# Kernel optimization log

Hardware: AMD Instinct MI355X
Metric: run time of the kernel (lower is better)

Reference implementation:

```python
import jax, jax.numpy as jnp
import numpy as np

V, E, H, T = 100000, 128, 256, 7
B, S = 64, 512
START, STOP = 5, 6
H2 = H // 2


def setup_inputs() -> dict:
    key = jax.random.key(0)
    ks = jax.random.split(key, 16)
    rn = lambda k, shape, s=0.1: jax.random.normal(k, shape, jnp.float32) * s
    inp = {}
    inp["sentence"] = jax.random.randint(ks[0], (B, S), 0, V)
    inp["tags"] = jax.random.randint(ks[1], (B, S), 0, 5)
    inp["h0"] = jax.random.normal(ks[2], (2, B, H2), jnp.float32)
    inp["c0"] = jax.random.normal(ks[3], (2, B, H2), jnp.float32)
    inp["embedding"] = rn(ks[4], (V, E), 1.0)
    inp["w_ih_f"] = rn(ks[5], (4 * H2, E)); inp["w_hh_f"] = rn(ks[6], (4 * H2, H2))
    inp["b_ih_f"] = rn(ks[7], (4 * H2,)); inp["b_hh_f"] = rn(ks[8], (4 * H2,))
    inp["w_ih_b"] = rn(ks[9], (4 * H2, E)); inp["w_hh_b"] = rn(ks[10], (4 * H2, H2))
    inp["b_ih_b"] = rn(ks[11], (4 * H2,)); inp["b_hh_b"] = rn(ks[12], (4 * H2,))
    inp["w_out"] = rn(ks[13], (T, H)); inp["b_out"] = rn(ks[14], (T,))
    trans = jax.random.normal(ks[15], (T, T), jnp.float32)
    trans = trans.at[START, :].set(-10000.0).at[:, STOP].set(-10000.0)
    inp["transitions"] = trans
    return inp


def _lstm_dir(x, h0, c0, wih, whh, bih, bhh, reverse):
    # x: [S, B, E]; PyTorch gate order i, f, g, o
    def step(carry, xt):
        h, c = carry
        z = xt @ wih.T + h @ whh.T + bih + bhh  # [B, 4*H2]
        i, f, g, o = jnp.split(z, 4, axis=-1)
        c = jax.nn.sigmoid(f) * c + jax.nn.sigmoid(i) * jnp.tanh(g)
        h = jax.nn.sigmoid(o) * jnp.tanh(c)
        return (h, c), h
    _, hs = jax.lax.scan(step, (h0, c0), x, reverse=reverse)
    return hs  # [S, B, H2]


def reference(sentence, tags, h0, c0, embedding, w_ih_f, w_hh_f, b_ih_f, b_hh_f,
              w_ih_b, w_hh_b, b_ih_b, b_hh_b, w_out, b_out, transitions):
    # Embedding; torch code does .view(S, B, -1) on a [B, S, E] tensor (raw
    # reinterpretation) -- replicate with reshape to match the math exactly.
    embeds = embedding[sentence].reshape(S, B, E)
    hf = _lstm_dir(embeds, h0[0], c0[0], w_ih_f, w_hh_f, b_ih_f, b_hh_f, False)
    hb = _lstm_dir(embeds, h0[1], c0[1], w_ih_b, w_hh_b, b_ih_b, b_hh_b, True)
    feats = jnp.concatenate([hf, hb], axis=-1) @ w_out.T + b_out  # [S, B, T]

    # CRF forward algorithm. Original uses transitions.t(), i.e. step score
    # for prev=i -> next=j is transitions[i, j].
    alpha0 = jnp.full((B, T), -10000.0, jnp.float32).at[:, START].set(0.0)
    def crf_step(alpha, feat):
        # [b, i, j]: alpha[b,i] + transitions[i,j]; LSE over i, add emit[b,j]
        a = jax.nn.logsumexp(alpha[:, :, None] + transitions[None, :, :], axis=1) + feat
        return a, None
    alpha, _ = jax.lax.scan(crf_step, alpha0, feats)
    fwd_score = jax.nn.logsumexp(alpha + transitions[STOP][None, :], axis=1)  # [B]

    # Gold path score: transitions[next, prev] + emit[next], per _score_sentence.
    tags_ext = jnp.concatenate([jnp.full((B, 1), START, tags.dtype), tags], axis=1)
    t_prev, t_next = tags_ext[:, :-1], tags_ext[:, 1:]  # [B, S]
    trans_sc = transitions[t_next, t_prev].sum(axis=1)
    emit_sc = jnp.take_along_axis(jnp.transpose(feats, (1, 0, 2)),
                                  t_next[:, :, None], axis=2)[..., 0].sum(axis=1)
    gold = trans_sc + emit_sc + transitions[STOP, tags_ext[:, -1]]
    return jnp.sum(fwd_score - gold) / B
```

## Files before the change

kernel.cpp:

```cpp
#include <hip/hip_runtime.h>

typedef unsigned int u32;
typedef unsigned short u16;
typedef __attribute__((ext_vector_type(8))) short short8;
typedef __attribute__((ext_vector_type(4))) float f32x4;

#define DEV __device__ __forceinline__
#define LOG2E 1.44269504089f

DEV u16 f2bf(float f) {
    u32 u = __float_as_uint(f);
    return (u16)((u + 0x7FFFu + ((u >> 16) & 1u)) >> 16);
}
DEV float bf2f(u16 h) { return __uint_as_float(((u32)h) << 16); }
DEV float frcp(float x) { return __builtin_amdgcn_rcpf(x); }
DEV float fexp2(float x) {
#if __has_builtin(__builtin_amdgcn_exp2f)
    return __builtin_amdgcn_exp2f(x);
#else
    return exp2f(x);
#endif
}
DEV u32 pack_bf16(float a, float b) {
#if __has_builtin(__builtin_amdgcn_cvt_pk_bf16_f32)
    auto v = __builtin_amdgcn_cvt_pk_bf16_f32(a, b);
    u32 r; __builtin_memcpy(&r, &v, 4); return r;
#else
    return (u32)f2bf(a) | ((u32)f2bf(b) << 16);
#endif
}
DEV float xex(uint2 v, int r) {
    u32 u = (r & 2) ? v.y : v.x;
    return (r & 1) ? __uint_as_float(u & 0xFFFF0000u) : __uint_as_float(u << 16);
}

__global__ __launch_bounds__(512) void k_inproj2(
    const int* __restrict__ sent, const float* __restrict__ emb,
    const float* __restrict__ wihf, const float* __restrict__ bihf, const float* __restrict__ bhhf,
    const float* __restrict__ wihb, const float* __restrict__ bihb, const float* __restrict__ bhhb,
    u16* __restrict__ Xf, u16* __restrict__ Xb)
{
    int blk = blockIdx.x;
    int d  = blk >> 8;
    int g4 = (blk >> 6) & 3;
    int sc = blk & 63;
    const float* wih = d ? wihb : wihf;
    const float* bih = d ? bihb : bihf;
    const float* bhh = d ? bhhb : bhhf;
    u16* X = d ? Xb : Xf;
    int tid = threadIdx.x;
    int w = tid >> 6, lane = tid & 63;
    int rg = lane >> 4, cn = lane & 15;

    short8 afr[4][4];
    #pragma unroll
    for (int mi = 0; mi < 4; ++mi) {
        int gate = 16 * (w + 8 * mi) + cn;
        #pragma unroll
        for (int kt = 0; kt < 4; ++kt) {
            const float* p = wih + (size_t)gate * 128 + kt * 32 + rg * 8;
            float4 f0 = *(const float4*)p;
            float4 f1 = *(const float4*)(p + 4);
            union { short8 v; u32 u[4]; } sv;
            sv.u[0] = pack_bf16(f0.x, f0.y);
            sv.u[1] = pack_bf16(f0.z, f0.w);
            sv.u[2] = pack_bf16(f1.x, f1.y);
            sv.u[3] = pack_bf16(f1.z, f1.w);
            afr[mi][kt] = sv.v;
        }
    }
    float bs[4][4];
    #pragma unroll
    for (int mi = 0; mi < 4; ++mi)
        #pragma unroll
        for (int r = 0; r < 4; ++r) {
            int g = 16 * (w + 8 * mi) + 4 * rg + r;
            bs[mi][r] = bih[g] + bhh[g];
        }

    __shared__ int toks[128];
    __shared__ u16 tile[8][16][136];
    if (tid < 128)
        toks[tid] = sent[(sc * 8 + (tid >> 4)) * 64 + g4 * 16 + (tid & 15)];
    __syncthreads();
    {
        int rr = tid >> 2, q = tid & 3;
        int ss = rr >> 4, nn = rr & 15;
        const float* er = emb + (size_t)toks[rr] * 128 + q * 32;
        u16* dst = &tile[ss][nn][q * 32];
        #pragma unroll
        for (int u = 0; u < 4; ++u) {
            float4 a = *(const float4*)(er + u * 8);
            float4 c = *(const float4*)(er + u * 8 + 4);
            uint4 st;
            st.x = pack_bf16(a.x, a.y); st.y = pack_bf16(a.z, a.w);
            st.z = pack_bf16(c.x, c.y); st.w = pack_bf16(c.z, c.w);
            *(uint4*)(dst + u * 8) = st;
        }
    }
    __syncthreads();

    for (int ss = 0; ss < 8; ++ss) {
        short8 bfr[4];
        #pragma unroll
        for (int kt = 0; kt < 4; ++kt)
            bfr[kt] = *(const short8*)&tile[ss][cn][kt * 32 + rg * 8];
        int s = sc * 8 + ss;
        #pragma unroll
        for (int mi = 0; mi < 4; ++mi) {
            f32x4 acc = {0.f, 0.f, 0.f, 0.f};
            #pragma unroll
            for (int kt = 0; kt < 4; ++kt)
                acc = __builtin_amdgcn_mfma_f32_16x16x32_bf16(afr[mi][kt], bfr[kt], acc, 0, 0, 0);
            size_t base = (((size_t)s * 4 + g4) * 32 + (w + 8 * mi)) * 256
                        + (size_t)rg * 64 + (size_t)cn * 4;
            uint2 st;
            st.x = pack_bf16((acc[0] + bs[mi][0]) * LOG2E, (acc[1] + bs[mi][1]) * LOG2E);
            st.y = pack_bf16((acc[2] + bs[mi][2]) * LOG2E, (acc[3] + bs[mi][3]) * LOG2E);
            *(uint2*)(X + base) = st;
        }
    }
}

__global__ __launch_bounds__(512) void k_lstm(
    const float* __restrict__ h0, const float* __restrict__ c0,
    const float* __restrict__ whhf, const float* __restrict__ whhb,
    const u16* __restrict__ Xf, const u16* __restrict__ Xb,
    u16* __restrict__ hfo, u16* __restrict__ hbo)
{
    int d  = blockIdx.x >> 2, g4 = blockIdx.x & 3;
    const float* whh = d ? whhb : whhf;
    const u16*   X   = d ? Xb   : Xf;
    u16*         ho  = d ? hbo  : hfo;
    int w = threadIdx.x >> 6, lane = threadIdx.x & 63;
    int rg = lane >> 4, cn = lane & 15;

    short8 afr[4][4];
    #pragma unroll
    for (int mi = 0; mi < 4; ++mi) {
        int gate = 16 * (w + 8 * mi) + cn;
        #pragma unroll
        for (int kt = 0; kt < 4; ++kt) {
            const float* p = whh + (size_t)gate * 128 + kt * 32 + rg * 8;
            float4 f0 = *(const float4*)p;
            float4 f1 = *(const float4*)(p + 4);
            union { short8 v; u32 u[4]; } sv;
            sv.u[0] = pack_bf16(f0.x * LOG2E, f0.y * LOG2E);
            sv.u[1] = pack_bf16(f0.z * LOG2E, f0.w * LOG2E);
            sv.u[2] = pack_bf16(f1.x * LOG2E, f1.y * LOG2E);
            sv.u[3] = pack_bf16(f1.z * LOG2E, f1.w * LOG2E);
            afr[mi][kt] = sv.v;
        }
    }
    int b = g4 * 16 + cn;
    int chb = 16 * w + rg * 4;
    float cst[4];
    {
        float4 cv = *(const float4*)(c0 + ((size_t)d * 64 + b) * 128 + chb);
        cst[0]=cv.x; cst[1]=cv.y; cst[2]=cv.z; cst[3]=cv.w;
    }
    __shared__ u16 hbuf[2][16][136];
    {
        float4 hv = *(const float4*)(h0 + ((size_t)d * 64 + b) * 128 + chb);
        uint2 st0;
        st0.x = pack_bf16(hv.x, hv.y);
        st0.y = pack_bf16(hv.z, hv.w);
        *(uint2*)&hbuf[0][cn][chb] = st0;
    }
    __syncthreads();

    int s0 = d ? 511 : 0;
    const int sdelta = d ? -32768 : 32768;
    const ptrdiff_t hdelta = d ? -8192 : 8192;
    size_t lof = (size_t)rg * 64 + (size_t)cn * 4;

    const u16* pa[4]; const u16* pb[4];
    uint2 xA[4], xB[4];
    #pragma unroll
    for (int mi = 0; mi < 4; ++mi) {
        const u16* base = X + (((size_t)s0 * 4 + g4) * 32 + (w + 8 * mi)) * 256 + lof;
        xA[mi] = *(const uint2*)base;
        xB[mi] = *(const uint2*)(base + sdelta);
        pa[mi] = base + 2 * sdelta;
        pb[mi] = base + 3 * sdelta;
    }
    u16* hop = ho + ((size_t)s0 * 64 + b) * 128 + chb;

#define LSTM_STEP(RB, WB, XC, XP)                                            \
    do {                                                                     \
        short8 bfr[4];                                                       \
        _Pragma("unroll")                                                    \
        for (int kt = 0; kt < 4; ++kt)                                       \
            bfr[kt] = *(const short8*)&hbuf[RB][cn][kt * 32 + rg * 8];       \
        f32x4 z[4];                                                          \
        _Pragma("unroll")                                                    \
        for (int mi = 0; mi < 4; ++mi) {                                     \
            f32x4 acc;                                                       \
            acc[0] = xex(XC[mi], 0); acc[1] = xex(XC[mi], 1);                \
            acc[2] = xex(XC[mi], 2); acc[3] = xex(XC[mi], 3);                \
            _Pragma("unroll")                                                \
            for (int kt = 0; kt < 4; ++kt)                                   \
                acc = __builtin_amdgcn_mfma_f32_16x16x32_bf16(               \
                    afr[mi][kt], bfr[kt], acc, 0, 0, 0);                     \
            z[mi] = acc;                                                     \
            XC[mi] = *(const uint2*)XP[mi];                                  \
            XP[mi] += 2 * sdelta;                                            \
        }                                                                    \
        float hnew[4];                                                       \
        _Pragma("unroll")                                                    \
        for (int r = 0; r < 4; ++r) {                                        \
            float zi = z[0][r], zf = z[1][r], zg = z[2][r], zo = z[3][r];    \
            float ei = fexp2(-zi);                                           \
            float ef = fexp2(-zf);                                           \
            float eo = fexp2(-zo);                                           \
            float eg = fexp2(fminf(zg + zg, 115.f));                         \
            float A = 1.f + ei, F = 1.f + ef, G = eg + 1.f, O = 1.f + eo;    \
            float AG = A * G;                                                \
            float cc = (cst[r] * AG + (eg - 1.f) * F) * frcp(F * AG);        \
            cst[r] = cc;                                                     \
            float ec = fexp2(fminf(2.885390082f * cc, 115.f));               \
            hnew[r] = (ec - 1.f) * frcp(O * (ec + 1.f));                     \
        }                                                                    \
        uint2 st;                                                            \
        st.x = pack_bf16(hnew[0], hnew[1]);                                  \
        st.y = pack_bf16(hnew[2], hnew[3]);                                  \
        *(uint2*)&hbuf[WB][cn][chb] = st;                                    \
        *(uint2*)hop = st;                                                   \
        hop += hdelta;                                                       \
        asm volatile("s_waitcnt lgkmcnt(0)\n\ts_barrier" ::: "memory");      \
    } while (0)

    for (int it = 0; it < 256; ++it) {
        LSTM_STEP(0, 1, xA, pa);
        LSTM_STEP(1, 0, xB, pb);
    }
#undef LSTM_STEP
}

__global__ __launch_bounds__(256) void k_feats(
    const u16* __restrict__ hf, const u16* __restrict__ hb,
    const float* __restrict__ wout, const float* __restrict__ bout,
    float* __restrict__ feats)
{
    __shared__ u16 sf[32][136], sb[32][136];
    __shared__ float wo[7][260];
    __shared__ float bo[8];
    int tid = threadIdx.x;
    int pos0 = blockIdx.x * 32;
    {
        int r = tid >> 3, cc = (tid & 7) * 16;
        const uint4* pf = (const uint4*)(hf + (size_t)(pos0 + r) * 128 + cc);
        const uint4* pb = (const uint4*)(hb + (size_t)(pos0 + r) * 128 + cc);
        *(uint4*)&sf[r][cc]     = pf[0];
        *(uint4*)&sf[r][cc + 8] = pf[1];
        *(uint4*)&sb[r][cc]     = pb[0];
        *(uint4*)&sb[r][cc + 8] = pb[1];
    }
    for (int i = tid; i < 1792; i += 256) wo[i >> 8][i & 255] = wout[i];
    if (tid < 7) bo[tid] = bout[tid];
    __syncthreads();
    int pp = tid >> 3, tt = tid & 7;
    if (tt < 7) {
        float acc = bo[tt];
        #pragma unroll 4
        for (int ch = 0; ch < 128; ++ch)
            acc += bf2f(sf[pp][ch]) * wo[tt][ch]
                 + bf2f(sb[pp][ch]) * wo[tt][128 + ch];
        feats[(size_t)(pos0 + pp) * 7 + tt] = acc;
    }
}

__global__ __launch_bounds__(64) void k_crf_chunk(
    const float* __restrict__ feats, const float* __restrict__ trans,
    float* __restrict__ chunkM)
{
    int b = blockIdx.x >> 3, c = blockIdx.x & 7;
    int lane = threadIdx.x;
    int i = lane >> 3, j = lane & 7;
    __shared__ float M[8][8];
    __shared__ float fl[64][8];
    int s0 = c * 64;
    for (int idx = lane; idx < 448; idx += 64) {
        int ss = idx / 7, jj = idx - ss * 7;
        fl[ss][jj] = feats[(size_t)((s0 + ss) * 64 + b) * 7 + jj];
    }
    float tc[7];
    #pragma unroll
    for (int k = 0; k < 7; ++k) tc[k] = (j < 7) ? trans[k * 7 + j] : 0.f;
    __syncthreads();
    M[i][j] = (i < 7 && j < 7) ? (trans[i * 7 + j] + fl[0][j]) : -1e30f;
    __syncthreads();
    for (int ss = 1; ss < 64; ++ss) {
        float4 m0 = *(const float4*)&M[i][0];
        float4 m1 = *(const float4*)&M[i][4];
        float v0 = m0.x + tc[0], v1 = m0.y + tc[1], v2 = m0.z + tc[2];
        float v3 = m0.w + tc[3], v4 = m1.x + tc[4], v5 = m1.y + tc[5];
        float v6 = m1.z + tc[6];
        float mx = fmaxf(fmaxf(fmaxf(v0, v1), fmaxf(v2, v3)),
                         fmaxf(fmaxf(v4, v5), v6));
        float sm = __expf(v0 - mx) + __expf(v1 - mx) + __expf(v2 - mx)
                 + __expf(v3 - mx) + __expf(v4 - mx) + __expf(v5 - mx)
                 + __expf(v6 - mx);
        float r = mx + __logf(sm) + fl[ss][j];
        __syncthreads();
        if (i < 7 && j < 7) M[i][j] = r;
        __syncthreads();
    }
    if (i < 7 && j < 7)
        chunkM[(size_t)(b * 8 + c) * 49 + i * 7 + j] = M[i][j];
}

__global__ __launch_bounds__(64) void k_crf_final(
    const float* __restrict__ chunkM, const float* __restrict__ trans,
    const int* __restrict__ tags, const float* __restrict__ feats,
    float* __restrict__ out)
{
    int b = blockIdx.x;
    int lane = threadIdx.x;
    __shared__ float P[8][49];
    __shared__ float Tl[49];
    __shared__ float av[2][8];
    __shared__ int   tg[512];
    for (int idx = lane; idx < 392; idx += 64)
        P[idx / 49][idx % 49] = chunkM[(size_t)b * 392 + idx];
    if (lane < 49) Tl[lane] = trans[lane];
    for (int idx = lane; idx < 512; idx += 64) tg[idx] = tags[(size_t)b * 512 + idx];
    if (lane < 8) av[0][lane] = (lane == 5) ? 0.f : -1e4f;
    __syncthreads();
    int cur = 0;
    for (int cch = 0; cch < 8; ++cch) {
        if (lane < 7) {
            float vv[7], mx = -1e30f;
            #pragma unroll
            for (int ii = 0; ii < 7; ++ii) {
                vv[ii] = av[cur][ii] + P[cch][ii * 7 + lane];
                mx = fmaxf(mx, vv[ii]);
            }
            float sm = 0.f;
            #pragma unroll
            for (int ii = 0; ii < 7; ++ii) sm += __expf(vv[ii] - mx);
            av[cur ^ 1][lane] = mx + __logf(sm);
        }
        __syncthreads();
        cur ^= 1;
    }
    float mx = -1e30f, uu[7];
    #pragma unroll
    for (int jj = 0; jj < 7; ++jj) {
        uu[jj] = av[cur][jj] + Tl[6 * 7 + jj];
        mx = fmaxf(mx, uu[jj]);
    }
    float sm = 0.f;
    #pragma unroll
    for (int jj = 0; jj < 7; ++jj) sm += __expf(uu[jj] - mx);
    float fwd = mx + __logf(sm);
    float acc = 0.f;
    for (int ss = lane; ss < 512; ss += 64) {
        int tn = tg[ss];
        int tp = (ss == 0) ? 5 : tg[ss - 1];
        acc += Tl[tn * 7 + tp] + feats[(size_t)(ss * 64 + b) * 7 + tn];
    }
    #pragma unroll
    for (int mk = 32; mk >= 1; mk >>= 1) acc += __shfl_xor(acc, mk, 64);
    if (lane == 0) {
        float gold = acc + Tl[6 * 7 + tg[511]];
        atomicAdd(out, (fwd - gold) * (1.0f / 64.0f));
    }
}

extern "C" void kernel_launch(void* const* d_in, const int* in_sizes, int n_in,
                              void* d_out, int out_size, void* d_ws, size_t ws_size,
                              hipStream_t stream) {
    const int*   sent = (const int*)d_in[0];
    const int*   tags = (const int*)d_in[1];
    const float* h0   = (const float*)d_in[2];
    const float* c0   = (const float*)d_in[3];
    const float* emb  = (const float*)d_in[4];
    const float* wihf = (const float*)d_in[5];
    const float* whhf = (const float*)d_in[6];
    const float* bihf = (const float*)d_in[7];
    const float* bhhf = (const float*)d_in[8];
    const float* wihb = (const float*)d_in[9];
    const float* whhb = (const float*)d_in[10];
    const float* bihb = (const float*)d_in[11];
    const float* bhhb = (const float*)d_in[12];
    const float* wout = (const float*)d_in[13];
    const float* bout = (const float*)d_in[14];
    const float* trn  = (const float*)d_in[15];

    char* ws = (char*)d_ws;
    u16*   Xf     = (u16*)(ws);
    u16*   Xb     = (u16*)(ws + 33554432);
    u16*   hfp    = (u16*)(ws + 67108864);
    u16*   hbp    = (u16*)(ws + 75497472);
    float* feats  = (float*)(ws + 83886080);
    float* chunkM = (float*)(ws + 84803584);

    hipMemsetAsync(d_out, 0, 4, stream);
    k_inproj2<<<512, 512, 0, stream>>>(sent, emb, wihf, bihf, bhhf,
                                       wihb, bihb, bhhb, Xf, Xb);
    k_lstm<<<8, 512, 0, stream>>>(h0, c0, whhf, whhb, Xf, Xb, hfp, hbp);
    k_feats<<<1024, 256, 0, stream>>>(hfp, hbp, wout, bout, feats);
    k_crf_chunk<<<512, 64, 0, stream>>>(feats, trn, chunkM);
    k_crf_final<<<64, 64, 0, stream>>>(chunkM, trn, tags, feats, (float*)d_out);
}
```

Before: 576.8 us.

## Widen input-projection tiles to all batch columns and use scalar-base addressing in LSTM

The input projection kernel now has each block handle four timesteps across all 64 batch columns, in two staged 2-step shared tiles, instead of 8 timesteps for a 16-column group. This halves the grid so each block's W_ih fragment load and bf16 conversion is amortised over more MFMA work. The LSTM recurrence now uses a uniform scalar base pointer plus per-lane 32-bit offsets instead of per-lane 64-bit pointers, to cut address arithmetic and VGPR use on the serial critical path. The clamp limits and a couple of FMA contractions in the gate math are also tweaked. The risks are fewer blocks on the GPU and an extra barrier in the projection kernel.

```diff
diff --git a/kernel.cpp b/kernel.cpp
--- a/kernel.cpp
+++ b/kernel.cpp
@@ -41,9 +41,8 @@
     u16* __restrict__ Xf, u16* __restrict__ Xb)
 {
     int blk = blockIdx.x;
-    int d  = blk >> 8;
-    int g4 = (blk >> 6) & 3;
-    int sc = blk & 63;
+    int d  = blk >> 7;
+    int sc = blk & 127;
     const float* wih = d ? wihb : wihf;
     const float* bih = d ? bihb : bihf;
     const float* bhh = d ? bhhb : bhhf;
@@ -78,46 +77,50 @@
             bs[mi][r] = bih[g] + bhh[g];
         }
 
-    __shared__ int toks[128];
-    __shared__ u16 tile[8][16][136];
-    if (tid < 128)
-        toks[tid] = sent[(sc * 8 + (tid >> 4)) * 64 + g4 * 16 + (tid & 15)];
-    __syncthreads();
-    {
-        int rr = tid >> 2, q = tid & 3;
-        int ss = rr >> 4, nn = rr & 15;
-        const float* er = emb + (size_t)toks[rr] * 128 + q * 32;
-        u16* dst = &tile[ss][nn][q * 32];
+    __shared__ u16 tile[2][64][136];
+    #pragma unroll
+    for (int stage = 0; stage < 2; ++stage) {
+        if (stage) __syncthreads();
+        {
+            int row = tid >> 2, q = tid & 3;
+            int sl = row >> 6, bb = row & 63;
+            int tok = sent[(sc * 4 + stage * 2 + sl) * 64 + bb];
+            const float* er = emb + (size_t)tok * 128 + q * 32;
+            u16* dst = &tile[sl][bb][q * 32];
+            #pragma unroll
+            for (int u = 0; u < 4; ++u) {
+                float4 a = *(const float4*)(er + u * 8);
+                float4 c = *(const float4*)(er + u * 8 + 4);
+                uint4 st;
+                st.x = pack_bf16(a.x, a.y); st.y = pack_bf16(a.z, a.w);
+                st.z = pack_bf16(c.x, c.y); st.w = pack_bf16(c.z, c.w);
+                *(uint4*)(dst + u * 8) = st;
+            }
+        }
+        __syncthreads();
         #pragma unroll
-        for (int u = 0; u < 4; ++u) {
-            float4 a = *(const float4*)(er + u * 8);
-            float4 c = *(const float4*)(er + u * 8 + 4);
-            uint4 st;
-            st.x = pack_bf16(a.x, a.y); st.y = pack_bf16(a.z, a.w);
-            st.z = pack_bf16(c.x, c.y); st.w = pack_bf16(c.z, c.w);
-            *(uint4*)(dst + u * 8) = st;
-        }
-    }
-    __syncthreads();
-
-    for (int ss = 0; ss < 8; ++ss) {
-        short8 bfr[4];
-        #pragma unroll
-        for (int kt = 0; kt < 4; ++kt)
-            bfr[kt] = *(const short8*)&tile[ss][cn][kt * 32 + rg * 8];
-        int s = sc * 8 + ss;
-        #pragma unroll
-        for (int mi = 0; mi < 4; ++mi) {
-            f32x4 acc = {0.f, 0.f, 0.f, 0.f};
+        for (int ss = 0; ss < 2; ++ss) {
+            int s = sc * 4 + stage * 2 + ss;
             #pragma unroll
-            for (int kt = 0; kt < 4; ++kt)
-                acc = __builtin_amdgcn_mfma_f32_16x16x32_bf16(afr[mi][kt], bfr[kt], acc, 0, 0, 0);
-            size_t base = (((size_t)s * 4 + g4) * 32 + (w + 8 * mi)) * 256
-                        + (size_t)rg * 64 + (size_t)cn * 4;
-            uint2 st;
-            st.x = pack_bf16((acc[0] + bs[mi][0]) * LOG2E, (acc[1] + bs[mi][1]) * LOG2E);
-            st.y = pack_bf16((acc[2] + bs[mi][2]) * LOG2E, (acc[3] + bs[mi][3]) * LOG2E);
-            *(uint2*)(X + base) = st;
+            for (int nt = 0; nt < 4; ++nt) {
+                short8 bfr[4];
+                #pragma unroll
+                for (int kt = 0; kt < 4; ++kt)
+                    bfr[kt] = *(const short8*)&tile[ss][nt * 16 + cn][kt * 32 + rg * 8];
+                #pragma unroll
+                for (int mi = 0; mi < 4; ++mi) {
+                    f32x4 acc = {0.f, 0.f, 0.f, 0.f};
+                    #pragma unroll
+                    for (int kt = 0; kt < 4; ++kt)
+                        acc = __builtin_amdgcn_mfma_f32_16x16x32_bf16(afr[mi][kt], bfr[kt], acc, 0, 0, 0);
+                    size_t base = (((size_t)s * 4 + nt) * 32 + (w + 8 * mi)) * 256
+                                + (size_t)rg * 64 + (size_t)cn * 4;
+                    uint2 st;
+                    st.x = pack_bf16((acc[0] + bs[mi][0]) * LOG2E, (acc[1] + bs[mi][1]) * LOG2E);
+                    st.y = pack_bf16((acc[2] + bs[mi][2]) * LOG2E, (acc[3] + bs[mi][3]) * LOG2E);
+                    *(uint2*)(X + base) = st;
+                }
+            }
         }
     }
 }
@@ -170,23 +173,26 @@
     __syncthreads();
 
     int s0 = d ? 511 : 0;
-    const int sdelta = d ? -32768 : 32768;
-    const ptrdiff_t hdelta = d ? -8192 : 8192;
-    size_t lof = (size_t)rg * 64 + (size_t)cn * 4;
-
-    const u16* pa[4]; const u16* pb[4];
+    const int sdB = d ? -65536 : 65536;
+    const int hdB = d ? -16384 : 16384;
+
+    int voffB[4];
+    #pragma unroll
+    for (int mi = 0; mi < 4; ++mi)
+        voffB[mi] = 2 * ((w + 8 * mi) * 256 + rg * 64 + cn * 4);
+    const char* xbase = (const char*)X + ((size_t)s0 * 32768 + (size_t)g4 * 8192) * 2;
     uint2 xA[4], xB[4];
     #pragma unroll
     for (int mi = 0; mi < 4; ++mi) {
-        const u16* base = X + (((size_t)s0 * 4 + g4) * 32 + (w + 8 * mi)) * 256 + lof;
-        xA[mi] = *(const uint2*)base;
-        xB[mi] = *(const uint2*)(base + sdelta);
-        pa[mi] = base + 2 * sdelta;
-        pb[mi] = base + 3 * sdelta;
-    }
-    u16* hop = ho + ((size_t)s0 * 64 + b) * 128 + chb;
-
-#define LSTM_STEP(RB, WB, XC, XP)                                            \
+        xA[mi] = *(const uint2*)(xbase + voffB[mi]);
+        xB[mi] = *(const uint2*)(xbase + sdB + voffB[mi]);
+    }
+    const char* sxA = xbase + 2 * sdB;
+    const char* sxB = xbase + 3 * sdB;
+    int vhoff = 2 * (b * 128 + chb);
+    char* hsp = (char*)ho + (size_t)s0 * 16384;
+
+#define LSTM_STEP(RB, WB, XC, SX)                                            \
     do {                                                                     \
         short8 bfr[4];                                                       \
         _Pragma("unroll")                                                    \
@@ -203,9 +209,9 @@
                 acc = __builtin_amdgcn_mfma_f32_16x16x32_bf16(               \
                     afr[mi][kt], bfr[kt], acc, 0, 0, 0);                     \
             z[mi] = acc;                                                     \
-            XC[mi] = *(const uint2*)XP[mi];                                  \
-            XP[mi] += 2 * sdelta;                                            \
+            XC[mi] = *(const uint2*)(SX + voffB[mi]);                        \
         }                                                                    \
+        SX += 2 * sdB;                                                       \
         float hnew[4];                                                       \
         _Pragma("unroll")                                                    \
         for (int r = 0; r < 4; ++r) {                                        \
@@ -213,26 +219,27 @@
             float ei = fexp2(-zi);                                           \
             float ef = fexp2(-zf);                                           \
             float eo = fexp2(-zo);                                           \
-            float eg = fexp2(fminf(zg + zg, 115.f));                         \
-            float A = 1.f + ei, F = 1.f + ef, G = eg + 1.f, O = 1.f + eo;    \
+            float eg = fexp2(fminf(zg + zg, 126.f));                         \
+            float A = 1.f + ei, F = 1.f + ef, G = 1.f + eg, O = 1.f + eo;    \
             float AG = A * G;                                                \
-            float cc = (cst[r] * AG + (eg - 1.f) * F) * frcp(F * AG);        \
+            float num = fmaf(cst[r], AG, (eg - 1.f) * F);                    \
+            float cc  = num * frcp(F * AG);                                  \
             cst[r] = cc;                                                     \
-            float ec = fexp2(fminf(2.885390082f * cc, 115.f));               \
-            hnew[r] = (ec - 1.f) * frcp(O * (ec + 1.f));                     \
+            float ec = fexp2(fminf(2.885390082f * cc, 126.f));               \
+            hnew[r] = (ec - 1.f) * frcp(fmaf(O, ec, O));                     \
         }                                                                    \
         uint2 st;                                                            \
         st.x = pack_bf16(hnew[0], hnew[1]);                                  \
         st.y = pack_bf16(hnew[2], hnew[3]);                                  \
         *(uint2*)&hbuf[WB][cn][chb] = st;                                    \
-        *(uint2*)hop = st;                                                   \
-        hop += hdelta;                                                       \
+        *(uint2*)(hsp + vhoff) = st;                                         \
+        hsp += hdB;                                                          \
         asm volatile("s_waitcnt lgkmcnt(0)\n\ts_barrier" ::: "memory");      \
     } while (0)
 
     for (int it = 0; it < 256; ++it) {
-        LSTM_STEP(0, 1, xA, pa);
-        LSTM_STEP(1, 0, xB, pb);
+        LSTM_STEP(0, 1, xA, sxA);
+        LSTM_STEP(1, 0, xB, sxB);
     }
 #undef LSTM_STEP
 }
@@ -397,7 +404,7 @@
     float* chunkM = (float*)(ws + 84803584);
 
     hipMemsetAsync(d_out, 0, 4, stream);
-    k_inproj2<<<512, 512, 0, stream>>>(sent, emb, wihf, bihf, bhhf,
+    k_inproj2<<<256, 512, 0, stream>>>(sent, emb, wihf, bihf, bhhf,
                                        wihb, bihb, bhhb, Xf, Xb);
     k_lstm<<<8, 512, 0, stream>>>(h0, c0, whhf, whhb, Xf, Xb, hfp, hbp);
     k_feats<<<1024, 256, 0, stream>>>(hfp, hbp, wout, bout, feats);
```

Result: no change. 576.3 us (-0.1%).

## Retile input projection over full batch and fold CRF final into one block

Applied to the files above, without the earlier changes.

The input projection now has each block cover all 64 batch columns for 4 timesteps, in two staged halves, instead of 16 columns for 8 timesteps. This halves the grid and cuts how often each block's weight-fragment setup is repeated. The CRF final kernel becomes a single 512-thread block that runs all 64 batch rows with shuffles and reduces in shared memory, which removes the memset and the atomicAdd. The trade-off is fewer blocks for the projection and a serial per-thread gold-score loop over 64 steps. All of these kernels are small next to the sequential LSTM kernel.

```diff
diff --git a/kernel.cpp b/kernel.cpp
--- a/kernel.cpp
+++ b/kernel.cpp
@@ -41,9 +41,8 @@
     u16* __restrict__ Xf, u16* __restrict__ Xb)
 {
     int blk = blockIdx.x;
-    int d  = blk >> 8;
-    int g4 = (blk >> 6) & 3;
-    int sc = blk & 63;
+    int d  = blk >> 7;
+    int sc = blk & 127;
     const float* wih = d ? wihb : wihf;
     const float* bih = d ? bihb : bihf;
     const float* bhh = d ? bhhb : bhhf;
@@ -78,46 +77,50 @@
             bs[mi][r] = bih[g] + bhh[g];
         }
 
-    __shared__ int toks[128];
-    __shared__ u16 tile[8][16][136];
-    if (tid < 128)
-        toks[tid] = sent[(sc * 8 + (tid >> 4)) * 64 + g4 * 16 + (tid & 15)];
-    __syncthreads();
-    {
-        int rr = tid >> 2, q = tid & 3;
-        int ss = rr >> 4, nn = rr & 15;
-        const float* er = emb + (size_t)toks[rr] * 128 + q * 32;
-        u16* dst = &tile[ss][nn][q * 32];
-        #pragma unroll
-        for (int u = 0; u < 4; ++u) {
-            float4 a = *(const float4*)(er + u * 8);
-            float4 c = *(const float4*)(er + u * 8 + 4);
-            uint4 st;
-            st.x = pack_bf16(a.x, a.y); st.y = pack_bf16(a.z, a.w);
-            st.z = pack_bf16(c.x, c.y); st.w = pack_bf16(c.z, c.w);
-            *(uint4*)(dst + u * 8) = st;
-        }
-    }
-    __syncthreads();
-
-    for (int ss = 0; ss < 8; ++ss) {
-        short8 bfr[4];
-        #pragma unroll
-        for (int kt = 0; kt < 4; ++kt)
-            bfr[kt] = *(const short8*)&tile[ss][cn][kt * 32 + rg * 8];
-        int s = sc * 8 + ss;
-        #pragma unroll
-        for (int mi = 0; mi < 4; ++mi) {
-            f32x4 acc = {0.f, 0.f, 0.f, 0.f};
+    __shared__ u16 tile[2][64][136];
+    #pragma unroll
+    for (int stage = 0; stage < 2; ++stage) {
+        if (stage) __syncthreads();
+        {
+            int row = tid >> 2, q = tid & 3;
+            int sl = row >> 6, bb = row & 63;
+            int tok = sent[(sc * 4 + stage * 2 + sl) * 64 + bb];
+            const float* er = emb + (size_t)tok * 128 + q * 32;
+            u16* dst = &tile[sl][bb][q * 32];
             #pragma unroll
-            for (int kt = 0; kt < 4; ++kt)
-                acc = __builtin_amdgcn_mfma_f32_16x16x32_bf16(afr[mi][kt], bfr[kt], acc, 0, 0, 0);
-            size_t base = (((size_t)s * 4 + g4) * 32 + (w + 8 * mi)) * 256
-                        + (size_t)rg * 64 + (size_t)cn * 4;
-            uint2 st;
-            st.x = pack_bf16((acc[0] + bs[mi][0]) * LOG2E, (acc[1] + bs[mi][1]) * LOG2E);
-            st.y = pack_bf16((acc[2] + bs[mi][2]) * LOG2E, (acc[3] + bs[mi][3]) * LOG2E);
-            *(uint2*)(X + base) = st;
+            for (int u = 0; u < 4; ++u) {
+                float4 a = *(const float4*)(er + u * 8);
+                float4 c = *(const float4*)(er + u * 8 + 4);
+                uint4 st;
+                st.x = pack_bf16(a.x, a.y); st.y = pack_bf16(a.z, a.w);
+                st.z = pack_bf16(c.x, c.y); st.w = pack_bf16(c.z, c.w);
+                *(uint4*)(dst + u * 8) = st;
+            }
+        }
+        __syncthreads();
+        #pragma unroll
+        for (int ss = 0; ss < 2; ++ss) {
+            int s = sc * 4 + stage * 2 + ss;
+            #pragma unroll
+            for (int nt = 0; nt < 4; ++nt) {
+                short8 bfr[4];
+                #pragma unroll
+                for (int kt = 0; kt < 4; ++kt)
+                    bfr[kt] = *(const short8*)&tile[ss][nt * 16 + cn][kt * 32 + rg * 8];
+                #pragma unroll
+                for (int mi = 0; mi < 4; ++mi) {
+                    f32x4 acc = {0.f, 0.f, 0.f, 0.f};
+                    #pragma unroll
+                    for (int kt = 0; kt < 4; ++kt)
+                        acc = __builtin_amdgcn_mfma_f32_16x16x32_bf16(afr[mi][kt], bfr[kt], acc, 0, 0, 0);
+                    size_t base = (((size_t)s * 4 + nt) * 32 + (w + 8 * mi)) * 256
+                                + (size_t)rg * 64 + (size_t)cn * 4;
+                    uint2 st;
+                    st.x = pack_bf16((acc[0] + bs[mi][0]) * LOG2E, (acc[1] + bs[mi][1]) * LOG2E);
+                    st.y = pack_bf16((acc[2] + bs[mi][2]) * LOG2E, (acc[3] + bs[mi][3]) * LOG2E);
+                    *(uint2*)(X + base) = st;
+                }
+            }
         }
     }
 }
@@ -310,61 +313,79 @@
         chunkM[(size_t)(b * 8 + c) * 49 + i * 7 + j] = M[i][j];
 }
 
-__global__ __launch_bounds__(64) void k_crf_final(
+__global__ __launch_bounds__(512) void k_crf_final(
     const float* __restrict__ chunkM, const float* __restrict__ trans,
     const int* __restrict__ tags, const float* __restrict__ feats,
     float* __restrict__ out)
 {
-    int b = blockIdx.x;
-    int lane = threadIdx.x;
-    __shared__ float P[8][49];
+    int tid = threadIdx.x;
+    int w = tid >> 6, lane = tid & 63;
+    int k = lane >> 3, j = lane & 7;
+    int b = w * 8 + k;
+    bool jv = (j < 7);
     __shared__ float Tl[49];
-    __shared__ float av[2][8];
-    __shared__ int   tg[512];
-    for (int idx = lane; idx < 392; idx += 64)
-        P[idx / 49][idx % 49] = chunkM[(size_t)b * 392 + idx];
-    if (lane < 49) Tl[lane] = trans[lane];
-    for (int idx = lane; idx < 512; idx += 64) tg[idx] = tags[(size_t)b * 512 + idx];
-    if (lane < 8) av[0][lane] = (lane == 5) ? 0.f : -1e4f;
-    __syncthreads();
-    int cur = 0;
-    for (int cch = 0; cch < 8; ++cch) {
-        if (lane < 7) {
-            float vv[7], mx = -1e30f;
-            #pragma unroll
-            for (int ii = 0; ii < 7; ++ii) {
-                vv[ii] = av[cur][ii] + P[cch][ii * 7 + lane];
-                mx = fmaxf(mx, vv[ii]);
-            }
-            float sm = 0.f;
-            #pragma unroll
-            for (int ii = 0; ii < 7; ++ii) sm += __expf(vv[ii] - mx);
-            av[cur ^ 1][lane] = mx + __logf(sm);
-        }
-        __syncthreads();
-        cur ^= 1;
-    }
-    float mx = -1e30f, uu[7];
-    #pragma unroll
-    for (int jj = 0; jj < 7; ++jj) {
-        uu[jj] = av[cur][jj] + Tl[6 * 7 + jj];
-        mx = fmaxf(mx, uu[jj]);
-    }
-    float sm = 0.f;
-    #pragma unroll
-    for (int jj = 0; jj < 7; ++jj) sm += __expf(uu[jj] - mx);
-    float fwd = mx + __logf(sm);
+    __shared__ float red[512];
+    __shared__ float fsh[64];
+    if (tid < 49) Tl[tid] = trans[tid];
+    __syncthreads();
+
+    float av = (j == 5) ? 0.f : -1e4f;
+    #pragma unroll
+    for (int c = 0; c < 8; ++c) {
+        float a0 = __shfl(av, k * 8 + 0, 64);
+        float a1 = __shfl(av, k * 8 + 1, 64);
+        float a2 = __shfl(av, k * 8 + 2, 64);
+        float a3 = __shfl(av, k * 8 + 3, 64);
+        float a4 = __shfl(av, k * 8 + 4, 64);
+        float a5 = __shfl(av, k * 8 + 5, 64);
+        float a6 = __shfl(av, k * 8 + 6, 64);
+        if (jv) {
+            const float* Pp = chunkM + ((size_t)b * 8 + c) * 49 + j;
+            float v0 = a0 + Pp[0],  v1 = a1 + Pp[7],  v2 = a2 + Pp[14];
+            float v3 = a3 + Pp[21], v4 = a4 + Pp[28], v5 = a5 + Pp[35];
+            float v6 = a6 + Pp[42];
+            float mx = fmaxf(fmaxf(fmaxf(v0, v1), fmaxf(v2, v3)),
+                             fmaxf(fmaxf(v4, v5), v6));
+            float sm = __expf(v0 - mx) + __expf(v1 - mx) + __expf(v2 - mx)
+                     + __expf(v3 - mx) + __expf(v4 - mx) + __expf(v5 - mx)
+                     + __expf(v6 - mx);
+            av = mx + __logf(sm);
+        }
+    }
+    float u = jv ? (av + Tl[42 + j]) : -1e30f;
+    float m = u;
+    #pragma unroll
+    for (int off = 1; off < 8; off <<= 1) m = fmaxf(m, __shfl_xor(m, off, 64));
+    float e = jv ? __expf(u - m) : 0.f;
+    #pragma unroll
+    for (int off = 1; off < 8; off <<= 1) e += __shfl_xor(e, off, 64);
+    float fwd = m + __logf(e);
+    if (j == 0) fsh[b] = fwd;
+
+    int tb = tid & 63, q = tid >> 6;
+    const int* tgp = tags + (size_t)tb * 512;
     float acc = 0.f;
-    for (int ss = lane; ss < 512; ss += 64) {
-        int tn = tg[ss];
-        int tp = (ss == 0) ? 5 : tg[ss - 1];
-        acc += Tl[tn * 7 + tp] + feats[(size_t)(ss * 64 + b) * 7 + tn];
-    }
-    #pragma unroll
-    for (int mk = 32; mk >= 1; mk >>= 1) acc += __shfl_xor(acc, mk, 64);
-    if (lane == 0) {
-        float gold = acc + Tl[6 * 7 + tg[511]];
-        atomicAdd(out, (fwd - gold) * (1.0f / 64.0f));
+    int tp = (q == 0) ? 5 : tgp[q * 64 - 1];
+    for (int ss = q * 64; ss < q * 64 + 64; ++ss) {
+        int tn = tgp[ss];
+        acc += Tl[tn * 7 + tp] + feats[(size_t)(ss * 64 + tb) * 7 + tn];
+        tp = tn;
+    }
+    if (q == 7) acc += Tl[42 + tgp[511]];
+    red[tid] = acc;
+    __syncthreads();
+    if (tid < 64) {
+        float g = red[tid];
+        #pragma unroll
+        for (int qq = 1; qq < 8; ++qq) g += red[tid + 64 * qq];
+        red[tid] = fsh[tid] - g;
+    }
+    __syncthreads();
+    if (tid < 64) {
+        float v = red[tid];
+        #pragma unroll
+        for (int off = 1; off < 64; off <<= 1) v += __shfl_xor(v, off, 64);
+        if (tid == 0) out[0] = v * (1.0f / 64.0f);
     }
 }
 
@@ -396,11 +417,10 @@
     float* feats  = (float*)(ws + 83886080);
     float* chunkM = (float*)(ws + 84803584);
 
-    hipMemsetAsync(d_out, 0, 4, stream);
-    k_inproj2<<<512, 512, 0, stream>>>(sent, emb, wihf, bihf, bhhf,
+    k_inproj2<<<256, 512, 0, stream>>>(sent, emb, wihf, bihf, bhhf,
                                        wihb, bihb, bhhb, Xf, Xb);
     k_lstm<<<8, 512, 0, stream>>>(h0, c0, whhf, whhb, Xf, Xb, hfp, hbp);
     k_feats<<<1024, 256, 0, stream>>>(hfp, hbp, wout, bout, feats);
     k_crf_chunk<<<512, 64, 0, stream>>>(feats, trn, chunkM);
-    k_crf_final<<<64, 64, 0, stream>>>(chunkM, trn, tags, feats, (float*)d_out);
-}
+    k_crf_final<<<1, 512, 0, stream>>>(chunkM, trn, tags, feats, (float*)d_out);
+}
```

New measurement: 571.9 us. Within noise of the previous version (-0.9%).
